# Kernel optimization log

Measured on AMD Instinct MI355X. Metric: run time of the kernel, lower is better.

The kernel has to match this reference:

```python
import jax, jax.numpy as jnp
import numpy as np

N_NODES = 20000
N_EDGES = 320000
IN_CH = 256
HID_CH = 256   # 2 * out_channels
OUT_CH = 128


def gcn_conv(x, edge_index, W, b, n_nodes):
    """PyG GCNConv: linear transform, add self-loops, sym-normalized scatter-add."""
    x = x @ W  # [N, C_out]
    loop = jnp.arange(n_nodes, dtype=edge_index.dtype)
    row = jnp.concatenate([edge_index[0], loop])  # source nodes
    col = jnp.concatenate([edge_index[1], loop])  # destination nodes
    deg = jax.ops.segment_sum(jnp.ones_like(col, dtype=x.dtype), col,
                              num_segments=n_nodes)
    deg_inv_sqrt = jnp.where(deg > 0, jax.lax.rsqrt(deg), 0.0)
    norm = deg_inv_sqrt[row] * deg_inv_sqrt[col]  # [E+N]
    msg = x[row] * norm[:, None]                  # gather + scale
    out = jax.ops.segment_sum(msg, col, num_segments=n_nodes)  # scatter-add
    return out + b


def setup_inputs() -> dict:
    key = jax.random.key(0)
    k1, k2, k3, k4, k5 = jax.random.split(key, 5)
    doc_embeds = jax.random.normal(k1, (N_NODES, IN_CH), dtype=jnp.float32)
    edge_index = jax.random.randint(k2, (2, N_EDGES), 0, N_NODES, dtype=jnp.int64)
    # Glorot-style init for GCN weights, zero bias (PyG defaults)
    s1 = 1.0 / np.sqrt(IN_CH)
    s2 = 1.0 / np.sqrt(HID_CH)
    W1 = jax.random.uniform(k3, (IN_CH, HID_CH), jnp.float32, -s1, s1)
    b1 = jnp.zeros((HID_CH,), jnp.float32)
    W2 = jax.random.uniform(k4, (HID_CH, OUT_CH), jnp.float32, -s2, s2)
    b2 = jnp.zeros((OUT_CH,), jnp.float32)
    return {"doc_embeds": doc_embeds, "edge_index": edge_index,
            "W1": W1, "b1": b1, "W2": W2, "b2": b2}


def reference(doc_embeds, edge_index, W1, b1, W2, b2):
    n = doc_embeds.shape[0]
    x = jax.nn.relu(gcn_conv(doc_embeds, edge_index, W1, b1, n))
    x = gcn_conv(x, edge_index, W2, b2, n)
    return x
```

## Files before the change

### kernel.cpp

```cpp
#include <hip/hip_runtime.h>
#include <math.h>

#define N_NODES 20000
#define N_EDGES 320000
#define IN_CH   256
#define HID_CH  256
#define OUT_CH  128
#define CAP     64

typedef __attribute__((ext_vector_type(8))) short short8;
typedef __attribute__((ext_vector_type(8))) unsigned short ushort8;
typedef __attribute__((ext_vector_type(4))) unsigned short ushort4v;
typedef __attribute__((ext_vector_type(4))) float floatx4;
typedef __attribute__((ext_vector_type(4))) _Float16 half4;
typedef __attribute__((ext_vector_type(8))) _Float16 half8;

static __device__ __forceinline__ unsigned short f2bf(float f) {
    unsigned int u = __float_as_uint(f);
    u += 0x7FFFu + ((u >> 16) & 1u);
    return (unsigned short)(u >> 16);
}
static __device__ __forceinline__ float bf2f(unsigned short h) {
    return __uint_as_float(((unsigned int)h) << 16);
}

__global__ __launch_bounds__(256)
void init_kernel(const float* __restrict__ W1, const float* __restrict__ W2,
                 unsigned short* __restrict__ W1thi, unsigned short* __restrict__ W1tlo,
                 unsigned short* __restrict__ W2thi, unsigned short* __restrict__ W2tlo,
                 int* __restrict__ deg) {
    const int g = blockIdx.x * blockDim.x + threadIdx.x;
    const int gsz = gridDim.x * blockDim.x;
    for (int i = g; i < N_NODES; i += gsz) deg[i] = 0;
    for (int t = g; t < (IN_CH * HID_CH) / 16; t += gsz) {
        int n = t >> 4;
        int kc = (t & 15) * 16;
        ushort8 h0, l0, h1, l1;
#pragma unroll
        for (int j = 0; j < 8; ++j) {
            float x = W1[(size_t)(kc + j) * HID_CH + n];
            h0[j] = f2bf(x); l0[j] = f2bf(x - bf2f(h0[j]));
            float y = W1[(size_t)(kc + 8 + j) * HID_CH + n];
            h1[j] = f2bf(y); l1[j] = f2bf(y - bf2f(h1[j]));
        }
        *(ushort8*)(W1thi + (size_t)n * IN_CH + kc)     = h0;
        *(ushort8*)(W1thi + (size_t)n * IN_CH + kc + 8) = h1;
        *(ushort8*)(W1tlo + (size_t)n * IN_CH + kc)     = l0;
        *(ushort8*)(W1tlo + (size_t)n * IN_CH + kc + 8) = l1;
    }
    for (int t = g; t < (HID_CH * OUT_CH) / 16; t += gsz) {
        int n = t >> 4;
        int kc = (t & 15) * 16;
        ushort8 h0, l0, h1, l1;
#pragma unroll
        for (int j = 0; j < 8; ++j) {
            float x = W2[(size_t)(kc + j) * OUT_CH + n];
            h0[j] = f2bf(x); l0[j] = f2bf(x - bf2f(h0[j]));
            float y = W2[(size_t)(kc + 8 + j) * OUT_CH + n];
            h1[j] = f2bf(y); l1[j] = f2bf(y - bf2f(h1[j]));
        }
        *(ushort8*)(W2thi + (size_t)n * HID_CH + kc)     = h0;
        *(ushort8*)(W2thi + (size_t)n * HID_CH + kc + 8) = h1;
        *(ushort8*)(W2tlo + (size_t)n * HID_CH + kc)     = l0;
        *(ushort8*)(W2tlo + (size_t)n * HID_CH + kc + 8) = l1;
    }
}

__global__ void degfill_kernel(const int* __restrict__ row, const int* __restrict__ col,
                               int* __restrict__ deg, unsigned short* __restrict__ srcs, int E) {
    int i = blockIdx.x * blockDim.x + threadIdx.x;
    if (i < E) {
        int c = col[i];
        int r = row[i];
        int p = atomicAdd(&deg[c], 1);
        srcs[(size_t)c * CAP + p] = (unsigned short)r;
    }
}

#define GK 256
template <int AMODE, int TM>
__global__ __launch_bounds__(256)
void gemm_mfma_kernel(const float* __restrict__ Afp, const _Float16* __restrict__ Ah,
                      const unsigned short* __restrict__ Bthi, const unsigned short* __restrict__ Btlo,
                      const int* __restrict__ deg, _Float16* __restrict__ C, int M, int N) {
    constexpr int MI = TM / 32;
    __shared__ unsigned short As[2][TM][36];
    __shared__ unsigned short Bs[2][128][36];
    const int tid = threadIdx.x;
    const int m0 = blockIdx.y * TM;
    const int n0 = blockIdx.x * 128;
    const int lane = tid & 63;
    const int wave = tid >> 6;
    const int wr = (wave >> 1) * (TM / 2);
    const int wc = (wave & 1) * 64;
    const int lm = lane & 15;
    const int lk = (lane >> 4) * 8;

    floatx4 acc[MI][4];
#pragma unroll
    for (int i = 0; i < MI; ++i)
#pragma unroll
        for (int j = 0; j < 4; ++j) acc[i][j] = (floatx4){0.f, 0.f, 0.f, 0.f};

    for (int k0 = 0; k0 < GK; k0 += 32) {
#pragma unroll
        for (int c = 0; c < TM / 64; ++c) {
            int ch = tid + c * 256;
            int r = ch >> 2;
            int ko = (ch & 3) * 8;
            ushort8 vh = {}, vl = {};
            if (m0 + r < M) {
                float xs[8];
                if (AMODE == 1) {
                    const float* ap = Afp + (size_t)(m0 + r) * GK + k0 + ko;
                    float4 f0 = *(const float4*)ap;
                    float4 f1 = *(const float4*)(ap + 4);
                    xs[0] = f0.x; xs[1] = f0.y; xs[2] = f0.z; xs[3] = f0.w;
                    xs[4] = f1.x; xs[5] = f1.y; xs[6] = f1.z; xs[7] = f1.w;
                } else {
                    half8 hv = *(const half8*)(Ah + (size_t)(m0 + r) * GK + k0 + ko);
#pragma unroll
                    for (int j = 0; j < 8; ++j) xs[j] = (float)hv[j];
                }
#pragma unroll
                for (int j = 0; j < 8; ++j) {
                    vh[j] = f2bf(xs[j]);
                    vl[j] = f2bf(xs[j] - bf2f(vh[j]));
                }
            }
            *(ushort8*)&As[0][r][ko] = vh;
            *(ushort8*)&As[1][r][ko] = vl;
        }
#pragma unroll
        for (int c = 0; c < 2; ++c) {
            int ch = tid + c * 256;
            int r = ch >> 2;
            int ko = (ch & 3) * 8;
            size_t gb = (size_t)(n0 + r) * GK + k0 + ko;
            *(ushort8*)&Bs[0][r][ko] = *(const ushort8*)(Bthi + gb);
            *(ushort8*)&Bs[1][r][ko] = *(const ushort8*)(Btlo + gb);
        }
        __syncthreads();

        short8 ah[MI], al[MI], bh[4], bl[4];
#pragma unroll
        for (int i = 0; i < MI; ++i) {
            ah[i] = *(const short8*)&As[0][wr + i * 16 + lm][lk];
            al[i] = *(const short8*)&As[1][wr + i * 16 + lm][lk];
        }
#pragma unroll
        for (int j = 0; j < 4; ++j) {
            bh[j] = *(const short8*)&Bs[0][wc + j * 16 + lm][lk];
            bl[j] = *(const short8*)&Bs[1][wc + j * 16 + lm][lk];
        }
#pragma unroll
        for (int i = 0; i < MI; ++i)
#pragma unroll
            for (int j = 0; j < 4; ++j) {
                acc[i][j] = __builtin_amdgcn_mfma_f32_16x16x32_bf16(ah[i], bh[j], acc[i][j], 0, 0, 0);
                acc[i][j] = __builtin_amdgcn_mfma_f32_16x16x32_bf16(ah[i], bl[j], acc[i][j], 0, 0, 0);
                acc[i][j] = __builtin_amdgcn_mfma_f32_16x16x32_bf16(al[i], bh[j], acc[i][j], 0, 0, 0);
            }
        __syncthreads();
    }

#pragma unroll
    for (int i = 0; i < MI; ++i) {
#pragma unroll
        for (int r = 0; r < 4; ++r) {
            int rowi = m0 + wr + i * 16 + (lane >> 4) * 4 + r;
            if (rowi < M) {
                float dr = 1.0f / sqrtf((float)(deg[rowi] + 1));
#pragma unroll
                for (int j = 0; j < 4; ++j) {
                    C[(size_t)rowi * N + n0 + wc + j * 16 + lm] = (_Float16)(dr * acc[i][j][r]);
                }
            }
        }
    }
}

template <int C, int NSLICE, int MODE>
__global__ __launch_bounds__(256)
void gather_sliced_kernel(const _Float16* __restrict__ X, const int* __restrict__ deg,
                          const unsigned short* __restrict__ srcs,
                          const float* __restrict__ bias, float* __restrict__ outf,
                          _Float16* __restrict__ outh, int n) {
    constexpr int SW = C / NSLICE;
    static_assert(SW == 32, "slice must be 32 channels");
    const int slice = blockIdx.x % NSLICE;
    const int ngrp  = blockIdx.x / NSLICE;
    const int wave = threadIdx.x >> 6;
    const int lane = threadIdx.x & 63;
    const int g  = lane >> 3;
    const int sl = lane & 7;
    const int node = ngrp * 32 + wave * 8 + g;
    if (node >= n) return;
    const int choff = slice * SW + sl * 4;
    const size_t beg = (size_t)node * CAP;
    const int cnt = deg[node];

    float4 acc = make_float4(0.f, 0.f, 0.f, 0.f);
    int e = 0;
    for (; e + 4 <= cnt; e += 4) {
        ushort4v s4 = *(const ushort4v*)(srcs + beg + e);
        half4 v0 = *(const half4*)(X + (size_t)s4.x * C + choff);
        half4 v1 = *(const half4*)(X + (size_t)s4.y * C + choff);
        half4 v2 = *(const half4*)(X + (size_t)s4.z * C + choff);
        half4 v3 = *(const half4*)(X + (size_t)s4.w * C + choff);
        acc.x += (float)v0.x + (float)v1.x + (float)v2.x + (float)v3.x;
        acc.y += (float)v0.y + (float)v1.y + (float)v2.y + (float)v3.y;
        acc.z += (float)v0.z + (float)v1.z + (float)v2.z + (float)v3.z;
        acc.w += (float)v0.w + (float)v1.w + (float)v2.w + (float)v3.w;
    }
    for (; e < cnt; ++e) {
        int r = srcs[beg + e];
        half4 v = *(const half4*)(X + (size_t)r * C + choff);
        acc.x += (float)v.x; acc.y += (float)v.y;
        acc.z += (float)v.z; acc.w += (float)v.w;
    }

    const float dc = 1.0f / sqrtf((float)(cnt + 1));
    half4 vsh = *(const half4*)(X + (size_t)node * C + choff);
    float4 bb = *(const float4*)(bias + choff);

    float o0 = dc * (acc.x + (float)vsh.x) + bb.x;
    float o1 = dc * (acc.y + (float)vsh.y) + bb.y;
    float o2 = dc * (acc.z + (float)vsh.z) + bb.z;
    float o3 = dc * (acc.w + (float)vsh.w) + bb.w;

    if constexpr (MODE == 1) {
        half4 h;
        h.x = (_Float16)fmaxf(o0, 0.f);
        h.y = (_Float16)fmaxf(o1, 0.f);
        h.z = (_Float16)fmaxf(o2, 0.f);
        h.w = (_Float16)fmaxf(o3, 0.f);
        *(half4*)(outh + (size_t)node * C + choff) = h;
    } else {
        floatx4 o = {o0, o1, o2, o3};
        __builtin_nontemporal_store(o, (floatx4*)(outf + (size_t)node * C + choff));
    }
}

extern "C" void kernel_launch(void* const* d_in, const int* in_sizes, int n_in,
                              void* d_out, int out_size, void* d_ws, size_t ws_size,
                              hipStream_t stream) {
    const float* doc_embeds = (const float*)d_in[0];
    const int*   edge_index = (const int*)d_in[1];
    const float* W1 = (const float*)d_in[2];
    const float* b1 = (const float*)d_in[3];
    const float* W2 = (const float*)d_in[4];
    const float* b2 = (const float*)d_in[5];
    float* out = (float*)d_out;

    const int* row = edge_index;
    const int* col = edge_index + N_EDGES;

    char* ws = (char*)d_ws;
    auto align_up = [](size_t x) { return (x + 255) / 256 * 256; };

    _Float16* X1s = (_Float16*)(ws);
    _Float16* H1  = (_Float16*)(ws + align_up((size_t)N_NODES * HID_CH * 2));
    _Float16* X2s = X1s;
    char* meta = (char*)(ws + 2 * align_up((size_t)N_NODES * HID_CH * 2));
    unsigned short* W1thi = (unsigned short*)(meta); meta += align_up((size_t)IN_CH * HID_CH * 2);
    unsigned short* W1tlo = (unsigned short*)(meta); meta += align_up((size_t)IN_CH * HID_CH * 2);
    unsigned short* W2thi = (unsigned short*)(meta); meta += align_up((size_t)HID_CH * OUT_CH * 2);
    unsigned short* W2tlo = (unsigned short*)(meta); meta += align_up((size_t)HID_CH * OUT_CH * 2);
    int*            deg   = (int*)(meta);            meta += align_up((size_t)N_NODES * 4);
    unsigned short* srcs  = (unsigned short*)(meta);

    init_kernel<<<256, 256, 0, stream>>>(W1, W2, W1thi, W1tlo, W2thi, W2tlo, deg);
    degfill_kernel<<<(N_EDGES + 255) / 256, 256, 0, stream>>>(row, col, deg, srcs, N_EDGES);

    {
        dim3 grid(HID_CH / 128, (N_NODES + 63) / 64);
        gemm_mfma_kernel<1, 64><<<grid, 256, 0, stream>>>(
            doc_embeds, nullptr, W1thi, W1tlo, deg, X1s, N_NODES, HID_CH);
    }
    gather_sliced_kernel<HID_CH, 8, 1><<<((N_NODES + 31) / 32) * 8, 256, 0, stream>>>(
        X1s, deg, srcs, b1, nullptr, H1, N_NODES);

    {
        dim3 grid(OUT_CH / 128, (N_NODES + 63) / 64);
        gemm_mfma_kernel<2, 64><<<grid, 256, 0, stream>>>(
            nullptr, H1, W2thi, W2tlo, deg, X2s, N_NODES, OUT_CH);
    }
    gather_sliced_kernel<OUT_CH, 4, 0><<<((N_NODES + 31) / 32) * 4, 256, 0, stream>>>(
        X2s, deg, srcs, b2, out, nullptr, N_NODES);
}
```

Baseline: 174.9 us.

## Merge weight prep with degree fill and narrow gather lanes to two channels

Merges the weight-splitting init kernel and the edge degree/CSR fill kernel into one launch, and zeroes the degree array with a memset issued before it. The gather kernel now maps 16 lanes per node with 2 channels each instead of 8 lanes with 4 channels, which doubles the block count and the number of independent gather loads in flight. This trades wider 8-byte loads for narrower 4-byte ones, adding more index loads and instructions per byte moved in exchange for more memory-level parallelism.

```diff
diff --git a/kernel.cpp b/kernel.cpp
--- a/kernel.cpp
+++ b/kernel.cpp
@@ -12,7 +12,9 @@
 typedef __attribute__((ext_vector_type(8))) unsigned short ushort8;
 typedef __attribute__((ext_vector_type(4))) unsigned short ushort4v;
 typedef __attribute__((ext_vector_type(4))) float floatx4;
+typedef __attribute__((ext_vector_type(2))) float floatx2;
 typedef __attribute__((ext_vector_type(4))) _Float16 half4;
+typedef __attribute__((ext_vector_type(2))) _Float16 half2v;
 typedef __attribute__((ext_vector_type(8))) _Float16 half8;
 
 static __device__ __forceinline__ unsigned short f2bf(float f) {
@@ -25,13 +27,13 @@
 }
 
 __global__ __launch_bounds__(256)
-void init_kernel(const float* __restrict__ W1, const float* __restrict__ W2,
+void prep_kernel(const float* __restrict__ W1, const float* __restrict__ W2,
                  unsigned short* __restrict__ W1thi, unsigned short* __restrict__ W1tlo,
                  unsigned short* __restrict__ W2thi, unsigned short* __restrict__ W2tlo,
-                 int* __restrict__ deg) {
+                 const int* __restrict__ row, const int* __restrict__ col,
+                 int* __restrict__ deg, unsigned short* __restrict__ srcs) {
     const int g = blockIdx.x * blockDim.x + threadIdx.x;
     const int gsz = gridDim.x * blockDim.x;
-    for (int i = g; i < N_NODES; i += gsz) deg[i] = 0;
     for (int t = g; t < (IN_CH * HID_CH) / 16; t += gsz) {
         int n = t >> 4;
         int kc = (t & 15) * 16;
@@ -64,12 +66,7 @@
         *(ushort8*)(W2tlo + (size_t)n * HID_CH + kc)     = l0;
         *(ushort8*)(W2tlo + (size_t)n * HID_CH + kc + 8) = l1;
     }
-}
-
-__global__ void degfill_kernel(const int* __restrict__ row, const int* __restrict__ col,
-                               int* __restrict__ deg, unsigned short* __restrict__ srcs, int E) {
-    int i = blockIdx.x * blockDim.x + threadIdx.x;
-    if (i < E) {
+    for (int i = g; i < N_EDGES; i += gsz) {
         int c = col[i];
         int r = row[i];
         int p = atomicAdd(&deg[c], 1);
@@ -192,53 +189,46 @@
     const int ngrp  = blockIdx.x / NSLICE;
     const int wave = threadIdx.x >> 6;
     const int lane = threadIdx.x & 63;
-    const int g  = lane >> 3;
-    const int sl = lane & 7;
-    const int node = ngrp * 32 + wave * 8 + g;
+    const int g  = lane >> 4;
+    const int sl = lane & 15;
+    const int node = ngrp * 16 + wave * 4 + g;
     if (node >= n) return;
-    const int choff = slice * SW + sl * 4;
+    const int choff = slice * SW + sl * 2;
     const size_t beg = (size_t)node * CAP;
     const int cnt = deg[node];
 
-    float4 acc = make_float4(0.f, 0.f, 0.f, 0.f);
+    float a0 = 0.f, a1 = 0.f;
     int e = 0;
     for (; e + 4 <= cnt; e += 4) {
         ushort4v s4 = *(const ushort4v*)(srcs + beg + e);
-        half4 v0 = *(const half4*)(X + (size_t)s4.x * C + choff);
-        half4 v1 = *(const half4*)(X + (size_t)s4.y * C + choff);
-        half4 v2 = *(const half4*)(X + (size_t)s4.z * C + choff);
-        half4 v3 = *(const half4*)(X + (size_t)s4.w * C + choff);
-        acc.x += (float)v0.x + (float)v1.x + (float)v2.x + (float)v3.x;
-        acc.y += (float)v0.y + (float)v1.y + (float)v2.y + (float)v3.y;
-        acc.z += (float)v0.z + (float)v1.z + (float)v2.z + (float)v3.z;
-        acc.w += (float)v0.w + (float)v1.w + (float)v2.w + (float)v3.w;
+        half2v v0 = *(const half2v*)(X + (size_t)s4.x * C + choff);
+        half2v v1 = *(const half2v*)(X + (size_t)s4.y * C + choff);
+        half2v v2 = *(const half2v*)(X + (size_t)s4.z * C + choff);
+        half2v v3 = *(const half2v*)(X + (size_t)s4.w * C + choff);
+        a0 += (float)v0.x + (float)v1.x + (float)v2.x + (float)v3.x;
+        a1 += (float)v0.y + (float)v1.y + (float)v2.y + (float)v3.y;
     }
     for (; e < cnt; ++e) {
         int r = srcs[beg + e];
-        half4 v = *(const half4*)(X + (size_t)r * C + choff);
-        acc.x += (float)v.x; acc.y += (float)v.y;
-        acc.z += (float)v.z; acc.w += (float)v.w;
+        half2v v = *(const half2v*)(X + (size_t)r * C + choff);
+        a0 += (float)v.x; a1 += (float)v.y;
     }
 
     const float dc = 1.0f / sqrtf((float)(cnt + 1));
-    half4 vsh = *(const half4*)(X + (size_t)node * C + choff);
-    float4 bb = *(const float4*)(bias + choff);
-
-    float o0 = dc * (acc.x + (float)vsh.x) + bb.x;
-    float o1 = dc * (acc.y + (float)vsh.y) + bb.y;
-    float o2 = dc * (acc.z + (float)vsh.z) + bb.z;
-    float o3 = dc * (acc.w + (float)vsh.w) + bb.w;
+    half2v vsh = *(const half2v*)(X + (size_t)node * C + choff);
+    float2 bb = *(const float2*)(bias + choff);
+
+    float o0 = dc * (a0 + (float)vsh.x) + bb.x;
+    float o1 = dc * (a1 + (float)vsh.y) + bb.y;
 
     if constexpr (MODE == 1) {
-        half4 h;
+        half2v h;
         h.x = (_Float16)fmaxf(o0, 0.f);
         h.y = (_Float16)fmaxf(o1, 0.f);
-        h.z = (_Float16)fmaxf(o2, 0.f);
-        h.w = (_Float16)fmaxf(o3, 0.f);
-        *(half4*)(outh + (size_t)node * C + choff) = h;
+        *(half2v*)(outh + (size_t)node * C + choff) = h;
     } else {
-        floatx4 o = {o0, o1, o2, o3};
-        __builtin_nontemporal_store(o, (floatx4*)(outf + (size_t)node * C + choff));
+        floatx2 o = {o0, o1};
+        __builtin_nontemporal_store(o, (floatx2*)(outf + (size_t)node * C + choff));
     }
 }
 
@@ -270,15 +260,16 @@
     int*            deg   = (int*)(meta);            meta += align_up((size_t)N_NODES * 4);
     unsigned short* srcs  = (unsigned short*)(meta);
 
-    init_kernel<<<256, 256, 0, stream>>>(W1, W2, W1thi, W1tlo, W2thi, W2tlo, deg);
-    degfill_kernel<<<(N_EDGES + 255) / 256, 256, 0, stream>>>(row, col, deg, srcs, N_EDGES);
+    hipMemsetAsync(deg, 0, (size_t)N_NODES * 4, stream);
+    prep_kernel<<<(N_EDGES + 255) / 256, 256, 0, stream>>>(
+        W1, W2, W1thi, W1tlo, W2thi, W2tlo, row, col, deg, srcs);
 
     {
         dim3 grid(HID_CH / 128, (N_NODES + 63) / 64);
         gemm_mfma_kernel<1, 64><<<grid, 256, 0, stream>>>(
             doc_embeds, nullptr, W1thi, W1tlo, deg, X1s, N_NODES, HID_CH);
     }
-    gather_sliced_kernel<HID_CH, 8, 1><<<((N_NODES + 31) / 32) * 8, 256, 0, stream>>>(
+    gather_sliced_kernel<HID_CH, 8, 1><<<((N_NODES + 15) / 16) * 8, 256, 0, stream>>>(
         X1s, deg, srcs, b1, nullptr, H1, N_NODES);
 
     {
@@ -286,6 +277,6 @@
         gemm_mfma_kernel<2, 64><<<grid, 256, 0, stream>>>(
             nullptr, H1, W2thi, W2tlo, deg, X2s, N_NODES, OUT_CH);
     }
-    gather_sliced_kernel<OUT_CH, 4, 0><<<((N_NODES + 31) / 32) * 4, 256, 0, stream>>>(
+    gather_sliced_kernel<OUT_CH, 4, 0><<<((N_NODES + 15) / 16) * 4, 256, 0, stream>>>(
         X2s, deg, srcs, b2, out, nullptr, N_NODES);
 }
```

Result: no change. 173.4 us (-0.8%).
